# Kernel optimization log

Measured on AMD Instinct MI355X. Metric: run time of the kernel, lower is better.

Reference implementation:

```python
import jax, jax.numpy as jnp
import numpy as np

IN_C, OUT_C, K, STRIDE, PAD = 16, 32, 3, 1, 1


def setup_inputs() -> dict:
    key = jax.random.key(0)
    kx, kw = jax.random.split(key)
    x = jax.random.normal(kx, (2, IN_C, 8, 8, 32, 32), dtype=jnp.float32)
    # matches torch.randn init of nn.Parameter
    weight = jax.random.normal(kw, (OUT_C, IN_C, K, K, K, K), dtype=jnp.float32)
    bias = jnp.zeros((OUT_C,), dtype=jnp.float32)
    return {"x": x, "weight": weight, "bias": bias}


def _conv4d(x, weight):
    # 4 spatial dims; layout N C T D H W, weight O I kT kD kH kW.
    dn = jax.lax.ConvDimensionNumbers(
        lhs_spec=(0, 1, 2, 3, 4, 5),
        rhs_spec=(0, 1, 2, 3, 4, 5),
        out_spec=(0, 1, 2, 3, 4, 5),
    )
    return jax.lax.conv_general_dilated(
        x, weight,
        window_strides=(STRIDE,) * 4,
        padding=((PAD, PAD),) * 4,
        dimension_numbers=dn,
    )


def reference(x, weight, bias):
    # Same math as unfold(im2col) + matmul + bias in the torch module,
    # expressed as a single N-D convolution (implicit GEMM).
    out = _conv4d(x, weight)  # [B, out_c, oT, oD, oH, oW]
    return out + bias[None, :, None, None, None, None]
```

## Files before the change

kernel.cpp:

```cpp
#include <hip/hip_runtime.h>

#define IN_C  16
#define OUT_C 32
#define NB 2
#define TT 8
#define DD 8
#define HH 32
#define WW 32
#define TP 10
#define DP 10
#define HP 34
#define WPAD 34

#define XT_ROW_B  1088
#define XT_ELEMS  (NB*TP*DP*HP*2*WPAD*8)
#define WT_TAPS_P 84
#define WT_ELEMS  (WT_TAPS_P*2*OUT_C*8)

#define A_SLAB_B 12288
#define B_CHUNK_B 28672

typedef __bf16 bf16x8 __attribute__((ext_vector_type(8)));
typedef float  f32x4  __attribute__((ext_vector_type(4)));
typedef float  f32x16 __attribute__((ext_vector_type(16)));

__device__ __forceinline__ unsigned short f2bf(float f) {
    unsigned int u = __builtin_bit_cast(unsigned int, f);
    u += 0x7fffu + ((u >> 16) & 1u);
    return (unsigned short)(u >> 16);
}

__device__ __forceinline__ void gload16(const void* g, void* l) {
    __builtin_amdgcn_global_load_lds(
        (const __attribute__((address_space(1))) unsigned int*)g,
        (__attribute__((address_space(3))) unsigned int*)l, 16, 0, 0);
}

__global__ __launch_bounds__(256) void prep_kernel(const float* __restrict__ x,
                                                   const float* __restrict__ wsrc,
                                                   unsigned short* __restrict__ xt,
                                                   unsigned short* __restrict__ wt) {
    int b = blockIdx.x;
    int tid = threadIdx.x;
    if (b < 4096) {
        __shared__ unsigned short ls[WW * IN_C];
        int h = b & 31, d = (b >> 5) & 7, t = (b >> 8) & 7, n = b >> 11;
        int c = tid >> 5, w = tid & 31;
        float v0 = x[((((size_t)(n * IN_C + c)     * TT + t) * DD + d) * HH + h) * WW + w];
        float v1 = x[((((size_t)(n * IN_C + c + 8) * TT + t) * DD + d) * HH + h) * WW + w];
        ls[w * 16 + c]     = f2bf(v0);
        ls[w * 16 + c + 8] = f2bf(v1);
        __syncthreads();
        if (tid < 68) {
            int blk = tid / 34, wl = tid % 34;
            unsigned char* row = (unsigned char*)xt +
                (size_t)(((n * TP + t + 1) * DP + d + 1) * HP + h + 1) * XT_ROW_B;
            f32x4 val = {0.f, 0.f, 0.f, 0.f};
            if (wl != 0 && wl != 33)
                val = *(const f32x4*)((const unsigned char*)ls + (wl - 1) * 32 + blk * 16);
            *(f32x4*)(row + tid * 16) = val;
        }
    } else if (b < 6800) {
        int j = b - 4096;
        int n, tp, dp, hp;
        if (j < 1360)      { n = j / 680;  int r = j % 680;  tp = (r / 340) * 9; int r2 = r % 340; dp = r2 / 34;       hp = r2 % 34; }
        else if (j < 2448) { int j2 = j - 1360; n = j2 / 544; int r = j2 % 544; tp = 1 + r / 68;  int r3 = r % 68;  dp = (r3 / 34) * 9; hp = r3 % 34; }
        else               { int j3 = j - 2448; n = j3 / 128; int r = j3 % 128; tp = 1 + r / 16;  int r4 = r % 16;  dp = 1 + r4 / 2;   hp = (r4 & 1) * 33; }
        if (tid < 68) {
            unsigned char* row = (unsigned char*)xt +
                (size_t)(((n * TP + tp) * DP + dp) * HP + hp) * XT_ROW_B;
            f32x4 z = {0.f, 0.f, 0.f, 0.f};
            *(f32x4*)(row + tid * 16) = z;
        }
    } else {
        int idx = (b - 6800) * 256 + tid;
        int tap = idx >> 9;
        int r = idx & 511;
        int icblk = r >> 8, oc = (r >> 3) & 31, i8 = r & 7;
        int ic = icblk * 8 + i8;
        float v = (tap < 81) ? wsrc[(oc * IN_C + ic) * 81 + tap] : 0.0f;
        wt[idx] = f2bf(v);
    }
}

__global__ __launch_bounds__(256, 2) void conv_main_kernel(const unsigned short* __restrict__ xt,
                                                           const unsigned short* __restrict__ wt,
                                                           const float* __restrict__ bias,
                                                           float* __restrict__ out) {
    __shared__ __align__(16) unsigned char As0[A_SLAB_B];
    __shared__ __align__(16) unsigned char As1[A_SLAB_B];
    __shared__ __align__(16) unsigned char Bs0[B_CHUNK_B];
    __shared__ __align__(16) unsigned char Bs1[B_CHUNK_B];

    int bid = blockIdx.x;
    int lb  = (bid & 7) * 64 + (bid >> 3);
    int hb = lb & 3, d = (lb >> 2) & 7, t = (lb >> 5) & 7, n = lb >> 8;
    int h0 = hb * 8;
    int tid  = threadIdx.x;
    int wv   = tid >> 6;
    int lane = tid & 63;
    int l31  = lane & 31;
    int kblk = lane >> 5;

    int ab = kblk * 544 + l31 * 16;
    int bb = kblk * 512 + l31 * 16;

#pragma unroll
    for (int i = 0; i < 7; ++i)
        gload16((const unsigned char*)wt + (tid + i * 256) * 16, Bs0 + (tid + i * 256) * 16);
    {
        const unsigned char* src = (const unsigned char*)xt +
            (size_t)(((n * TP + t) * DP + d) * HP + h0) * XT_ROW_B;
#pragma unroll
        for (int i = 0; i < 3; ++i)
            gload16(src + (tid + i * 256) * 16, As0 + (tid + i * 256) * 16);
    }
    asm volatile("s_waitcnt vmcnt(0)" ::: "memory");
    __syncthreads();

    f32x16 acc[4];
#pragma unroll
    for (int m = 0; m < 4; ++m) acc[m] = {};

#pragma unroll
    for (int p = 0; p < 9; ++p) {
        const int kt = p / 3, ph3 = p % 3;
        if (wv >= 2) {
            int tid2 = tid - 128;
            if (p < 8) {
                const int ktn = (p + 1) / 3, kdn = (p + 1) % 3;
                const unsigned char* src = (const unsigned char*)xt +
                    (size_t)(((n * TP + t + ktn) * DP + d + kdn) * HP + h0) * XT_ROW_B;
                unsigned char* dst = ((p + 1) & 1) ? As1 : As0;
#pragma unroll
                for (int i = 0; i < 6; ++i)
                    gload16(src + (tid2 + i * 128) * 16, dst + (tid2 + i * 128) * 16);
            }
            if (ph3 <= 1 && kt < 2) {
                int base = ph3 * 896;
                const unsigned char* bsrc = (const unsigned char*)wt +
                    (size_t)((kt + 1) * 27 * 64 + base) * 16;
                unsigned char* bdst = (((kt + 1) & 1) ? Bs1 : Bs0) + base * 16;
#pragma unroll
                for (int i = 0; i < 7; ++i)
                    gload16(bsrc + (tid2 + i * 128) * 16, bdst + (tid2 + i * 128) * 16);
            }
            asm volatile("s_waitcnt vmcnt(0)" ::: "memory");
        } else {
            const unsigned char* A = (p & 1) ? As1 : As0;
            const unsigned char* B = (kt & 1) ? Bs1 : Bs0;
            const int kd = ph3;

            bf16x8 bf[3][3];
#pragma unroll
            for (int kh = 0; kh < 3; ++kh)
#pragma unroll
                for (int kw = 0; kw < 3; ++kw)
                    bf[kh][kw] = *(const bf16x8*)(B + ((kd * 9 + kh * 3 + kw) << 10) + bb);

#pragma unroll
            for (int r = 0; r < 6; ++r) {
#pragma unroll
                for (int kw = 0; kw < 3; ++kw) {
                    bf16x8 a = *(const bf16x8*)(A + (4 * wv + r) * 1088 + ab + kw * 16);
#pragma unroll
                    for (int kh = 0; kh < 3; ++kh) {
                        const int m = r - kh;
                        if (m >= 0 && m < 4)
                            acc[m] = __builtin_amdgcn_mfma_f32_32x32x16_bf16(a, bf[kh][kw], acc[m], 0, 0, 0);
                    }
                }
            }
        }
        __syncthreads();
    }

    if (wv < 2) {
        float bsv = bias[l31];
#pragma unroll
        for (int m = 0; m < 4; ++m) {
            int oh = h0 + 4 * wv + m;
            float* obase = out + (((((size_t)n * OUT_C + l31) * TT + t) * DD + d) * HH + oh) * WW;
#pragma unroll
            for (int q = 0; q < 4; ++q) {
                f32x4 v = { acc[m][4 * q + 0] + bsv, acc[m][4 * q + 1] + bsv,
                            acc[m][4 * q + 2] + bsv, acc[m][4 * q + 3] + bsv };
                *(f32x4*)(obase + 8 * q + 4 * kblk) = v;
            }
        }
    }
}

extern "C" void kernel_launch(void* const* d_in, const int* in_sizes, int n_in,
                              void* d_out, int out_size, void* d_ws, size_t ws_size,
                              hipStream_t stream) {
    const float* x    = (const float*)d_in[0];
    const float* wsrc = (const float*)d_in[1];
    const float* bias = (const float*)d_in[2];
    float* out        = (float*)d_out;

    unsigned short* xt = (unsigned short*)d_ws;
    unsigned short* wt = xt + XT_ELEMS;

    prep_kernel<<<4096 + 2704 + 164, 256, 0, stream>>>(x, wsrc, xt, wt);
    conv_main_kernel<<<NB * TT * DD * 4, 256, 0, stream>>>(xt, wt, bias, out);
}
```

Measured before the change: 27.83 us.

## Replace producer/consumer warp split with all-waves compute and cooperative prefetch

Earlier, two waves only issued global-to-LDS loads and two waves ran all MFMAs, each owning four output rows. Now all four waves compute two output rows each and share the prefetch of the next A slab and B chunk. The wait before each barrier is relaxed to vmcnt(4) when a B chunk is in flight, so B loads for the next kt can stay outstanding while the next A slab is guaranteed. Doubling the MFMA-issuing waves should raise matrix-core use per block. In exchange each wave loads more A rows relative to the MFMAs it issues (4 rows for 2 outputs instead of 6 for 4), and every wave now stalls on its own loads.

```diff
diff --git a/kernel.cpp b/kernel.cpp
--- a/kernel.cpp
+++ b/kernel.cpp
@@ -118,75 +118,77 @@
     asm volatile("s_waitcnt vmcnt(0)" ::: "memory");
     __syncthreads();
 
-    f32x16 acc[4];
-#pragma unroll
-    for (int m = 0; m < 4; ++m) acc[m] = {};
+    f32x16 acc[2];
+    acc[0] = {}; acc[1] = {};
 
 #pragma unroll
     for (int p = 0; p < 9; ++p) {
         const int kt = p / 3, ph3 = p % 3;
-        if (wv >= 2) {
-            int tid2 = tid - 128;
-            if (p < 8) {
-                const int ktn = (p + 1) / 3, kdn = (p + 1) % 3;
-                const unsigned char* src = (const unsigned char*)xt +
-                    (size_t)(((n * TP + t + ktn) * DP + d + kdn) * HP + h0) * XT_ROW_B;
-                unsigned char* dst = ((p + 1) & 1) ? As1 : As0;
-#pragma unroll
-                for (int i = 0; i < 6; ++i)
-                    gload16(src + (tid2 + i * 128) * 16, dst + (tid2 + i * 128) * 16);
-            }
-            if (ph3 <= 1 && kt < 2) {
-                int base = ph3 * 896;
-                const unsigned char* bsrc = (const unsigned char*)wt +
-                    (size_t)((kt + 1) * 27 * 64 + base) * 16;
-                unsigned char* bdst = (((kt + 1) & 1) ? Bs1 : Bs0) + base * 16;
-#pragma unroll
-                for (int i = 0; i < 7; ++i)
-                    gload16(bsrc + (tid2 + i * 128) * 16, bdst + (tid2 + i * 128) * 16);
-            }
-            asm volatile("s_waitcnt vmcnt(0)" ::: "memory");
-        } else {
-            const unsigned char* A = (p & 1) ? As1 : As0;
-            const unsigned char* B = (kt & 1) ? Bs1 : Bs0;
-            const int kd = ph3;
-
-            bf16x8 bf[3][3];
-#pragma unroll
-            for (int kh = 0; kh < 3; ++kh)
-#pragma unroll
-                for (int kw = 0; kw < 3; ++kw)
-                    bf[kh][kw] = *(const bf16x8*)(B + ((kd * 9 + kh * 3 + kw) << 10) + bb);
-
-#pragma unroll
-            for (int r = 0; r < 6; ++r) {
-#pragma unroll
-                for (int kw = 0; kw < 3; ++kw) {
-                    bf16x8 a = *(const bf16x8*)(A + (4 * wv + r) * 1088 + ab + kw * 16);
-#pragma unroll
-                    for (int kh = 0; kh < 3; ++kh) {
-                        const int m = r - kh;
-                        if (m >= 0 && m < 4)
-                            acc[m] = __builtin_amdgcn_mfma_f32_32x32x16_bf16(a, bf[kh][kw], acc[m], 0, 0, 0);
-                    }
+
+        if (p < 8) {
+            const int ktn = (p + 1) / 3, kdn = (p + 1) % 3;
+            const unsigned char* src = (const unsigned char*)xt +
+                (size_t)(((n * TP + t + ktn) * DP + d + kdn) * HP + h0) * XT_ROW_B;
+            unsigned char* dst = ((p + 1) & 1) ? As1 : As0;
+#pragma unroll
+            for (int i = 0; i < 3; ++i)
+                gload16(src + (tid + i * 256) * 16, dst + (tid + i * 256) * 16);
+        }
+        const bool bstage = (kt < 2) && (ph3 <= 1);
+        if (bstage) {
+            const int basel = ph3 * 896;
+            const unsigned char* bsrc = (const unsigned char*)wt +
+                (size_t)((kt + 1) * 27 * 64 + basel) * 16;
+            unsigned char* bdst = (((kt + 1) & 1) ? Bs1 : Bs0) + basel * 16;
+#pragma unroll
+            for (int i = 0; i < 3; ++i)
+                gload16(bsrc + (tid + i * 256) * 16, bdst + (tid + i * 256) * 16);
+            if (tid < 128)
+                gload16(bsrc + (tid + 768) * 16, bdst + (tid + 768) * 16);
+        }
+
+        const unsigned char* A = (p & 1) ? As1 : As0;
+        const unsigned char* B = (kt & 1) ? Bs1 : Bs0;
+        const int kd = ph3;
+
+        bf16x8 bf[3][3];
+#pragma unroll
+        for (int kh = 0; kh < 3; ++kh)
+#pragma unroll
+            for (int kw = 0; kw < 3; ++kw)
+                bf[kh][kw] = *(const bf16x8*)(B + ((kd * 9 + kh * 3 + kw) << 10) + bb);
+
+#pragma unroll
+        for (int rr = 0; rr < 4; ++rr) {
+#pragma unroll
+            for (int kw = 0; kw < 3; ++kw) {
+                bf16x8 a = *(const bf16x8*)(A + (2 * wv + rr) * 1088 + ab + kw * 16);
+#pragma unroll
+                for (int kh = 0; kh < 3; ++kh) {
+                    const int m = rr - kh;
+                    if (m >= 0 && m < 2)
+                        acc[m] = __builtin_amdgcn_mfma_f32_32x32x16_bf16(a, bf[kh][kw], acc[m], 0, 0, 0);
                 }
             }
         }
+
+        if (bstage)
+            asm volatile("s_waitcnt vmcnt(4)" ::: "memory");
+        else
+            asm volatile("s_waitcnt vmcnt(0)" ::: "memory");
         __syncthreads();
     }
 
-    if (wv < 2) {
-        float bsv = bias[l31];
-#pragma unroll
-        for (int m = 0; m < 4; ++m) {
-            int oh = h0 + 4 * wv + m;
-            float* obase = out + (((((size_t)n * OUT_C + l31) * TT + t) * DD + d) * HH + oh) * WW;
-#pragma unroll
-            for (int q = 0; q < 4; ++q) {
-                f32x4 v = { acc[m][4 * q + 0] + bsv, acc[m][4 * q + 1] + bsv,
-                            acc[m][4 * q + 2] + bsv, acc[m][4 * q + 3] + bsv };
-                *(f32x4*)(obase + 8 * q + 4 * kblk) = v;
-            }
+    float bsv = bias[l31];
+#pragma unroll
+    for (int m = 0; m < 2; ++m) {
+        int oh = h0 + 2 * wv + m;
+        float* obase = out + (((((size_t)n * OUT_C + l31) * TT + t) * DD + d) * HH + oh) * WW;
+#pragma unroll
+        for (int q = 0; q < 4; ++q) {
+            f32x4 v = { acc[m][4 * q + 0] + bsv, acc[m][4 * q + 1] + bsv,
+                        acc[m][4 * q + 2] + bsv, acc[m][4 * q + 3] + bsv };
+            *(f32x4*)(obase + 8 * q + 4 * kblk) = v;
         }
     }
 }
```

New measurement: 26.55 us. 4.6% less time.
